# Kernel optimization log

Hardware: AMD Instinct MI355X
Metric: run time of the kernel (lower is better)

Reference implementation:

```python
import jax, jax.numpy as jnp
import numpy as np

N = 6144      # num_sample / nodes per graph
E = 196608    # edges per graph (avg degree 32)
F = 256       # input feature dim (same for all 4 graphs)
H = 256       # hidden_channels (== F so all SAGEConv layers are HxH)
D = 512       # fusion dim (hardcoded in module)
G = 4         # number of graphs
ATT = 128     # attention bottleneck (hardcoded)
WS = 0.05     # weight init scale


def setup_inputs() -> dict:
    key = jax.random.key(0)
    k = jax.random.split(key, 16)
    return {
        "xs": jax.random.normal(k[0], (G, N, F), jnp.float32),
        "edge_index": jax.random.randint(k[1], (G, 2, E), 0, N),
        "x_content": jax.random.normal(k[2], (N, F), jnp.float32),
        # SAGEConv params: per graph, 3 layers, lin_l (with bias) on aggregated
        # neighbors, lin_r (no bias) on root. F == H so all layers stack.
        "sage_Wl": jax.random.normal(k[3], (G, 3, H, H), jnp.float32) * WS,
        "sage_bl": jnp.zeros((G, 3, H), jnp.float32),
        "sage_Wr": jax.random.normal(k[4], (G, 3, H, H), jnp.float32) * WS,
        # lin1..lin4 : F -> 512
        "lin_W": jax.random.normal(k[5], (G, D, F), jnp.float32) * WS,
        "lin_b": jnp.zeros((G, D), jnp.float32),
        # ResidualFusion attention MLP 512 -> 128 -> 1, softmax over graph axis
        "att_W1": jax.random.normal(k[6], (ATT, D), jnp.float32) * WS,
        "att_b1": jnp.zeros((ATT,), jnp.float32),
        "att_W2": jax.random.normal(k[7], (1, ATT), jnp.float32) * WS,
        "att_b2": jnp.zeros((1,), jnp.float32),
        "res_W": jax.random.normal(k[8], (D, D), jnp.float32) * WS,
        "res_b": jnp.zeros((D,), jnp.float32),
        "fusion_weight": jnp.array([0.7, 0.3], jnp.float32),
        # SelfExpression coefficients, init 1e-8 * ones as in the module
        "C_content": jnp.full((N, N), 1e-8, jnp.float32),
        "C_structure": jnp.full((N, N), 1e-8, jnp.float32),
    }


def _gnn(x, ei, Wl, bl, Wr):
    # One GraphSAGE stack: 3 SAGEConv(mean) layers, relu after each,
    # dropout is identity in eval mode.
    src, dst = ei[0], ei[1]
    deg = jax.ops.segment_sum(jnp.ones((E,), x.dtype), dst, num_segments=N)
    deg = jnp.maximum(deg, 1.0)[:, None]
    for i in range(3):
        m = jax.ops.segment_sum(x[src], dst, num_segments=N) / deg  # mean aggr
        x = jax.nn.relu(m @ Wl[i].T + bl[i] + x @ Wr[i].T)
    return x


def reference(xs, edge_index, x_content, sage_Wl, sage_bl, sage_Wr,
              lin_W, lin_b, att_W1, att_b1, att_W2, att_b2,
              res_W, res_b, fusion_weight, C_content, C_structure):
    # Four GraphSAGE stacks, vmapped over the graph axis.
    xg = jax.vmap(_gnn)(xs, edge_index, sage_Wl, sage_bl, sage_Wr)  # [G,N,F]
    # lin1..lin4 -> [G,N,D]
    feats = jnp.einsum('gnf,gdf->gnd', xg, lin_W) + lin_b[:, None, :]
    # ResidualFusion: attention over stacked features, softmax over graph axis
    h = jax.nn.relu(jnp.einsum('gnd,kd->gnk', feats, att_W1) + att_b1)
    logits = jnp.einsum('gnk,ok->gno', h, att_W2) + att_b2  # [G,N,1]
    w = jax.nn.softmax(logits, axis=0)
    weighted = jnp.sum(w * feats, axis=0)            # [N,D]
    residual = feats[0] @ res_W.T + res_b            # [N,D]
    structure_features = jax.nn.relu(weighted + residual)
    # Coefficient fusion with softmax-normalized scalar weights
    fw = jax.nn.softmax(fusion_weight)
    fusion_expression = fw[0] * C_content + fw[1] * C_structure  # [N,N]
    return (fusion_expression, x_content, structure_features, C_content, C_structure)
```

## Files before the change

### kernel.cpp

```cpp
#include <hip/hip_runtime.h>
#include <hip/hip_bf16.h>

constexpr int N_ = 6144;
constexpr int E_ = 196608;
constexpr int F_ = 256;
constexpr int D_ = 512;
constexpr int G_ = 4;
constexpr int A_ = 128;

typedef short bf16x8 __attribute__((ext_vector_type(8)));
typedef float f32x4 __attribute__((ext_vector_type(4)));
typedef float f4 __attribute__((ext_vector_type(4)));
typedef int i4 __attribute__((ext_vector_type(4)));
typedef __hip_bfloat16 hb;

__device__ inline float b2f(unsigned short u) {
    union { unsigned u32; float f; } x; x.u32 = ((unsigned)u) << 16; return x.f;
}
__device__ inline unsigned short f2bu(float f) {
    hb b = __float2bfloat16(f);
    return *reinterpret_cast<unsigned short*>(&b);
}

#define GLD_LDS16(gp, lp) \
    __builtin_amdgcn_global_load_lds((const __attribute__((address_space(1))) void*)(gp), \
                                     (__attribute__((address_space(3))) void*)(lp), 16, 0, 0)

struct SP {
    const f4* Cc; const f4* Cs; const float* fw;
    f4* o0; f4* o3; f4* o4;
    long ib; long ie; int nsb;
};

__device__ void stream_slice(const SP sp, int sb)
{
    float fa = sp.fw[0], fb = sp.fw[1];
    float mx = fmaxf(fa, fb);
    float ea = expf(fa - mx), eb = expf(fb - mx);
    float w0 = ea / (ea + eb), w1 = eb / (ea + eb);
    const long S = (long)sp.nsb * blockDim.x;
    long i = sp.ib + (long)sb * blockDim.x + threadIdx.x;
    for (; i + 3 * S < sp.ie; i += 4 * S) {
        f4 a0 = __builtin_nontemporal_load(sp.Cc + i);
        f4 b0 = __builtin_nontemporal_load(sp.Cs + i);
        f4 a1 = __builtin_nontemporal_load(sp.Cc + i + S);
        f4 b1 = __builtin_nontemporal_load(sp.Cs + i + S);
        f4 a2 = __builtin_nontemporal_load(sp.Cc + i + 2 * S);
        f4 b2 = __builtin_nontemporal_load(sp.Cs + i + 2 * S);
        f4 a3 = __builtin_nontemporal_load(sp.Cc + i + 3 * S);
        f4 b3 = __builtin_nontemporal_load(sp.Cs + i + 3 * S);
        __builtin_nontemporal_store(a0, sp.o3 + i);
        __builtin_nontemporal_store(b0, sp.o4 + i);
        __builtin_nontemporal_store(w0 * a0 + w1 * b0, sp.o0 + i);
        __builtin_nontemporal_store(a1, sp.o3 + i + S);
        __builtin_nontemporal_store(b1, sp.o4 + i + S);
        __builtin_nontemporal_store(w0 * a1 + w1 * b1, sp.o0 + i + S);
        __builtin_nontemporal_store(a2, sp.o3 + i + 2 * S);
        __builtin_nontemporal_store(b2, sp.o4 + i + 2 * S);
        __builtin_nontemporal_store(w0 * a2 + w1 * b2, sp.o0 + i + 2 * S);
        __builtin_nontemporal_store(a3, sp.o3 + i + 3 * S);
        __builtin_nontemporal_store(b3, sp.o4 + i + 3 * S);
        __builtin_nontemporal_store(w0 * a3 + w1 * b3, sp.o0 + i + 3 * S);
    }
    for (; i < sp.ie; i += S) {
        f4 a = __builtin_nontemporal_load(sp.Cc + i);
        f4 b = __builtin_nontemporal_load(sp.Cs + i);
        __builtin_nontemporal_store(a, sp.o3 + i);
        __builtin_nontemporal_store(b, sp.o4 + i);
        __builtin_nontemporal_store(w0 * a + w1 * b, sp.o0 + i);
    }
}

__global__ void k_tail(SP sp) { stream_slice(sp, blockIdx.x); }

__global__ void k_prep(const float* __restrict__ xc, f4* __restrict__ o1,
                       const float* __restrict__ xs, ushort4* __restrict__ xsb,
                       const float* __restrict__ Wl, ushort4* __restrict__ Wlb,
                       const float* __restrict__ Wr, ushort4* __restrict__ Wrb,
                       const float* __restrict__ lin, ushort4* __restrict__ linb,
                       const float* __restrict__ aw, ushort4* __restrict__ awb,
                       const float* __restrict__ rw, ushort4* __restrict__ rwb,
                       i4* __restrict__ cursz, int PB, SP sp)
{
    if ((int)blockIdx.x < sp.nsb) { stream_slice(sp, blockIdx.x); return; }
    const int cb = blockIdx.x - sp.nsb;
    const long nz = (long)G_ * N_ / 4;
    const long n0 = (long)N_ * F_ / 4;
    const long n1 = (long)G_ * N_ * F_ / 4;
    const long n2 = (long)G_ * 3 * F_ * F_ / 4;
    const long n4 = (long)G_ * D_ * F_ / 4;
    const long n5 = (long)A_ * D_ / 4;
    const long n6 = (long)D_ * D_ / 4;
    const long T = nz + n0 + n1 + 2 * n2 + n4 + n5 + n6;
    long stride = (long)PB * blockDim.x;
    for (long u = (long)cb * blockDim.x + threadIdx.x; u < T; u += stride) {
        long v = u;
        if (v < nz) { cursz[v] = i4{0, 0, 0, 0}; continue; }
        v -= nz;
        if (v < n0) {
            f4 x = __builtin_nontemporal_load((const f4*)xc + v);
            __builtin_nontemporal_store(x, o1 + v);
            continue;
        }
        v -= n0;
        const float* s; ushort4* d;
        if (v < n1) { s = xs; d = xsb; }
        else {
            v -= n1;
            if (v < n2) { s = Wl; d = Wlb; }
            else {
                v -= n2;
                if (v < n2) { s = Wr; d = Wrb; }
                else {
                    v -= n2;
                    if (v < n4) { s = lin; d = linb; }
                    else {
                        v -= n4;
                        if (v < n5) { s = aw; d = awb; }
                        else { v -= n5; s = rw; d = rwb; }
                    }
                }
            }
        }
        f4 x = *((const f4*)s + v);
        ushort4 o;
        o.x = f2bu(x[0]); o.y = f2bu(x[1]); o.z = f2bu(x[2]); o.w = f2bu(x[3]);
        d[v] = o;
    }
}

__global__ void k_count(const int* __restrict__ ei, int* __restrict__ cnt, SP sp)
{
    if ((int)blockIdx.x < sp.nsb) { stream_slice(sp, blockIdx.x); return; }
    long i = (long)(blockIdx.x - sp.nsb) * blockDim.x + threadIdx.x;
    int g = (int)(i / E_);
    int e = (int)(i % E_);
    int dst = ei[(long)g * 2 * E_ + E_ + e];
    atomicAdd(&cnt[g * N_ + dst], 1);
}

__global__ void k_scan(int* __restrict__ cnt_cursor, int* __restrict__ row_ptr,
                       float* __restrict__ deg, SP sp)
{
    if ((int)blockIdx.x < sp.nsb) { stream_slice(sp, blockIdx.x); return; }
    int g = blockIdx.x - sp.nsb;
    __shared__ int sdata[1024];
    __shared__ int s_off;
    if (threadIdx.x == 0) s_off = 0;
    __syncthreads();
    for (int base = 0; base < N_; base += 1024) {
        int idx = g * N_ + base + threadIdx.x;
        int v = cnt_cursor[idx];
        sdata[threadIdx.x] = v;
        __syncthreads();
        for (int d = 1; d < 1024; d <<= 1) {
            int t = (threadIdx.x >= d) ? sdata[threadIdx.x - d] : 0;
            __syncthreads();
            sdata[threadIdx.x] += t;
            __syncthreads();
        }
        int incl = sdata[threadIdx.x];
        int excl = incl - v;
        int rp = s_off + excl;
        row_ptr[g * (N_ + 1) + base + threadIdx.x] = rp;
        cnt_cursor[idx] = rp;
        deg[idx] = (float)(v > 1 ? v : 1);
        __syncthreads();
        if (threadIdx.x == 1023) s_off += incl;
        __syncthreads();
    }
    if (threadIdx.x == 0) row_ptr[g * (N_ + 1) + N_] = s_off;
}

__global__ void k_fill(const int* __restrict__ ei, int* __restrict__ cursor,
                       int* __restrict__ csr_src, SP sp)
{
    if ((int)blockIdx.x < sp.nsb) { stream_slice(sp, blockIdx.x); return; }
    long i = (long)(blockIdx.x - sp.nsb) * blockDim.x + threadIdx.x;
    int g = (int)(i / E_);
    int e = (int)(i % E_);
    int src = ei[(long)g * 2 * E_ + e];
    int dst = ei[(long)g * 2 * E_ + E_ + e];
    int pos = atomicAdd(&cursor[g * N_ + dst], 1);
    csr_src[(long)g * E_ + pos] = src;
}

__global__ __launch_bounds__(256) void k_aggregate(
    const hb* __restrict__ x, const int* __restrict__ csr_src,
    const int* __restrict__ row_ptr, const float* __restrict__ deg,
    hb* __restrict__ m, SP sp)
{
    if ((int)blockIdx.x < sp.nsb) { stream_slice(sp, blockIdx.x); return; }
    int b = blockIdx.x - sp.nsb;
    int g = (b & 7) >> 1;
    int idx = ((b >> 3) << 1) | (b & 1);
    int node = idx * 4 + (threadIdx.x >> 6);
    int lane = threadIdx.x & 63;
    int qq = lane >> 4;
    int l16 = (lane & 15) * 16;
    const hb* xg = x + (long)g * N_ * F_;
    const int* rp = row_ptr + g * (N_ + 1);
    const int* cs = csr_src + (long)g * E_;
    int s = __builtin_amdgcn_readfirstlane(rp[node]);
    int e = __builtin_amdgcn_readfirstlane(rp[node + 1]);
    float a[16] = {};
    #pragma unroll 2
    for (int j = s; j < e; j += 4) {
        if (j + qq < e) {
            int src = cs[j + qq];
            const bf16x8* p = (const bf16x8*)(xg + (long)src * F_ + l16);
            bf16x8 v0 = p[0], v1 = p[1];
            #pragma unroll
            for (int q = 0; q < 8; ++q) a[q]     += b2f((unsigned short)v0[q]);
            #pragma unroll
            for (int q = 0; q < 8; ++q) a[q + 8] += b2f((unsigned short)v1[q]);
        }
    }
    #pragma unroll
    for (int q = 0; q < 16; ++q) {
        a[q] += __shfl_xor(a[q], 16);
        a[q] += __shfl_xor(a[q], 32);
    }
    if (qq == 0) {
        float inv = 1.0f / deg[g * N_ + node];
        bf16x8 lo, hi;
        #pragma unroll
        for (int q = 0; q < 8; ++q) { lo[q] = (short)f2bu(a[q] * inv); hi[q] = (short)f2bu(a[q + 8] * inv); }
        *(bf16x8*)(m + ((long)g * N_ + node) * F_ + l16) = lo;
        *(bf16x8*)(m + ((long)g * N_ + node) * F_ + l16 + 8) = hi;
    }
}

template <bool DUAL, bool RELU, bool LOGITS, bool FUSEOUT, bool PIN>
__global__ __launch_bounds__(256) void k_mfma_nt(
    const hb* __restrict__ A1, const hb* __restrict__ B1,
    const hb* __restrict__ A2, const hb* __restrict__ B2,
    const float* __restrict__ bias, hb* __restrict__ C,
    int ncols, int nrows, int ng, int Nc, int K,
    long a_batch, long b_batch, long bias_batch, long c_batch,
    const float* __restrict__ W2, const float* __restrict__ b2,
    float* __restrict__ logits,
    const float* __restrict__ lgAll, const hb* __restrict__ fAll,
    float* __restrict__ o2,
    SP sp)
{
    if ((int)blockIdx.x < sp.nsb) { stream_slice(sp, blockIdx.x); return; }
    int b = blockIdx.x - sp.nsb;
    int g, col, row;
    if (PIN) {
        g = (b & 7) >> 1;
        int idx = ((b >> 3) << 1) | (b & 1);
        col = idx % ncols; row = idx / ncols;
    } else {
        col = b % ncols;
        int r2 = b / ncols;
        row = r2 % nrows; g = r2 / nrows;
    }
    const int row0 = row * 128;
    const int col0 = col * 128;

    const hb* A1p = A1 + (long)g * a_batch;
    const hb* B1p = B1 + (long)g * b_batch;
    const hb* A2p = nullptr;
    const hb* B2p = nullptr;
    if (DUAL) { A2p = A2 + (long)g * a_batch; B2p = B2 + (long)g * b_batch; }
    const float* biasp = bias + (long)g * bias_batch;
    hb* Cp = C + (long)g * c_batch;

    __shared__ hb As[128 * 64];
    __shared__ hb Bs[128 * 64];
    __shared__ float sLog[2][128];
    __shared__ float sW[128][4];

    const int tid = threadIdx.x;
    const int lane = tid & 63;
    const int wid = tid >> 6;
    const int wr = wid >> 1;
    const int wc = wid & 1;

    if (FUSEOUT) {
        if (tid < 128) {
            int rr = row0 + tid;
            float l0 = lgAll[rr], l1 = lgAll[N_ + rr], l2 = lgAll[2 * N_ + rr], l3 = lgAll[3 * N_ + rr];
            float mx = fmaxf(fmaxf(l0, l1), fmaxf(l2, l3));
            float e0 = expf(l0 - mx), e1 = expf(l1 - mx), e2 = expf(l2 - mx), e3 = expf(l3 - mx);
            float inv = 1.f / (e0 + e1 + e2 + e3);
            sW[tid][0] = e0 * inv; sW[tid][1] = e1 * inv;
            sW[tid][2] = e2 * inv; sW[tid][3] = e3 * inv;
        }
    }

    const int srow = tid >> 3;
    const int sk8  = (tid & 7) * 8;

    f32x4 acc[4][4] = {};

    const int fr  = lane & 15;
    const int fkq = (lane >> 4) * 8;

    const int npass = DUAL ? 2 : 1;
    for (int pass = 0; pass < npass; ++pass) {
        const hb* A = (DUAL && pass) ? A2p : A1p;
        const hb* B = (DUAL && pass) ? B2p : B1p;
        for (int k0 = 0; k0 < K; k0 += 64) {
            __syncthreads();
            #pragma unroll
            for (int c = 0; c < 4; ++c) {
                int r = c * 32 + srow;
                GLD_LDS16(A + (long)(row0 + r) * K + k0 + sk8, As + r * 64 + sk8);
                GLD_LDS16(B + (long)(col0 + r) * K + k0 + sk8, Bs + r * 64 + sk8);
            }
            __syncthreads();

            bf16x8 af[4][2], bfr[4][2];
            #pragma unroll
            for (int m = 0; m < 4; ++m)
                #pragma unroll
                for (int kk = 0; kk < 2; ++kk)
                    af[m][kk] = *(const bf16x8*)(As + (wr * 64 + m * 16 + fr) * 64 + kk * 32 + fkq);
            #pragma unroll
            for (int n = 0; n < 4; ++n)
                #pragma unroll
                for (int kk = 0; kk < 2; ++kk)
                    bfr[n][kk] = *(const bf16x8*)(Bs + (wc * 64 + n * 16 + fr) * 64 + kk * 32 + fkq);

            #pragma unroll
            for (int m = 0; m < 4; ++m)
                #pragma unroll
                for (int n = 0; n < 4; ++n)
                    #pragma unroll
                    for (int kk = 0; kk < 2; ++kk)
                        acc[m][n] = __builtin_amdgcn_mfma_f32_16x16x32_bf16(
                            af[m][kk], bfr[n][kk], acc[m][n], 0, 0, 0);
        }
    }

    const int r4 = (lane >> 4) * 4;
    const int cc = lane & 15;

    if (LOGITS) {
        float w2v[4], bv[4];
        #pragma unroll
        for (int n = 0; n < 4; ++n) {
            int c2 = wc * 64 + n * 16 + cc;
            w2v[n] = W2[c2];
            bv[n]  = biasp[c2];
        }
        #pragma unroll
        for (int m = 0; m < 4; ++m) {
            #pragma unroll
            for (int j = 0; j < 4; ++j) {
                float p = 0.f;
                #pragma unroll
                for (int n = 0; n < 4; ++n) {
                    float h = fmaxf(acc[m][n][j] + bv[n], 0.f);
                    p += h * w2v[n];
                }
                p += __shfl_xor(p, 1); p += __shfl_xor(p, 2);
                p += __shfl_xor(p, 4); p += __shfl_xor(p, 8);
                if (cc == 0) sLog[wc][wr * 64 + m * 16 + r4 + j] = p;
            }
        }
        __syncthreads();
        if (tid < 128)
            logits[(long)g * N_ + row0 + tid] = sLog[0][tid] + sLog[1][tid] + b2[0];
    } else if (FUSEOUT) {
        const unsigned short* fu = (const unsigned short*)fAll;
        #pragma unroll
        for (int m = 0; m < 4; ++m) {
            #pragma unroll
            for (int n = 0; n < 4; ++n) {
                int c2 = col0 + wc * 64 + n * 16 + cc;
                float bv = biasp[c2];
                #pragma unroll
                for (int j = 0; j < 4; ++j) {
                    int rl = wr * 64 + m * 16 + r4 + j;
                    int rr = row0 + rl;
                    float s = acc[m][n][j] + bv;
                    #pragma unroll
                    for (int gg = 0; gg < 4; ++gg)
                        s += sW[rl][gg] * b2f(fu[((long)gg * N_ + rr) * D_ + c2]);
                    __builtin_nontemporal_store(fmaxf(s, 0.f), o2 + (long)rr * D_ + c2);
                }
            }
        }
    } else {
        #pragma unroll
        for (int m = 0; m < 4; ++m) {
            #pragma unroll
            for (int n = 0; n < 4; ++n) {
                int c2 = col0 + wc * 64 + n * 16 + cc;
                float bv = biasp[c2];
                #pragma unroll
                for (int j = 0; j < 4; ++j) {
                    int rr = row0 + wr * 64 + m * 16 + r4 + j;
                    float v = acc[m][n][j] + bv;
                    if (RELU) v = fmaxf(v, 0.f);
                    Cp[(long)rr * Nc + c2] = __float2bfloat16(v);
                }
            }
        }
    }
}

extern "C" void kernel_launch(void* const* d_in, const int* in_sizes, int n_in,
                              void* d_out, int out_size, void* d_ws, size_t ws_size,
                              hipStream_t stream)
{
    const float* xs        = (const float*)d_in[0];
    const int*   ei        = (const int*)  d_in[1];
    const float* x_content = (const float*)d_in[2];
    const float* sage_Wl   = (const float*)d_in[3];
    const float* sage_bl   = (const float*)d_in[4];
    const float* sage_Wr   = (const float*)d_in[5];
    const float* lin_W     = (const float*)d_in[6];
    const float* lin_b     = (const float*)d_in[7];
    const float* att_W1    = (const float*)d_in[8];
    const float* att_b1    = (const float*)d_in[9];
    const float* att_W2    = (const float*)d_in[10];
    const float* att_b2    = (const float*)d_in[11];
    const float* res_W     = (const float*)d_in[12];
    const float* res_b     = (const float*)d_in[13];
    const float* fusion_w  = (const float*)d_in[14];
    const float* Cc        = (const float*)d_in[15];
    const float* Cs        = (const float*)d_in[16];

    float* out0 = (float*)d_out;
    float* out1 = out0 + (size_t)N_ * N_;
    float* out2 = out1 + (size_t)N_ * F_;
    float* out3 = out2 + (size_t)N_ * D_;
    float* out4 = out3 + (size_t)N_ * N_;

    char* w = (char*)d_ws;
    auto alloc = [&](size_t bytes) {
        char* p = w;
        w += (bytes + 255) & ~(size_t)255;
        return p;
    };
    hb* xsb   = (hb*)alloc((size_t)G_ * N_ * F_ * 2);
    hb* xA    = (hb*)alloc((size_t)G_ * N_ * F_ * 2);
    hb* xB    = (hb*)alloc((size_t)G_ * N_ * F_ * 2);
    hb* mb    = (hb*)alloc((size_t)G_ * N_ * F_ * 2);
    hb* feats = (hb*)alloc((size_t)G_ * N_ * D_ * 2);
    hb* Wlb   = (hb*)alloc((size_t)G_ * 3 * F_ * F_ * 2);
    hb* Wrb   = (hb*)alloc((size_t)G_ * 3 * F_ * F_ * 2);
    hb* linWb = (hb*)alloc((size_t)G_ * D_ * F_ * 2);
    hb* attWb = (hb*)alloc((size_t)A_ * D_ * 2);
    hb* resWb = (hb*)alloc((size_t)D_ * D_ * 2);
    float* logit = (float*)alloc((size_t)G_ * N_ * 4);
    float* deg   = (float*)alloc((size_t)G_ * N_ * 4);
    int*   rowp  = (int*)  alloc((size_t)G_ * (N_ + 1) * 4);
    int*   curs  = (int*)  alloc((size_t)G_ * N_ * 4);
    int*   csrc  = (int*)  alloc((size_t)G_ * E_ * 4);

    const long U = (long)N_ * N_ / 4;
    const int cum[14] = {0, 85, 115, 135, 175, 285, 360, 470, 545, 655, 730, 820, 870, 975};
    long B[14];
    for (int i = 0; i < 14; ++i) B[i] = U * cum[i] / 1000;
    const int PREPB   = 512;
    const int SB_PREP = 512;
    const int SB_FLAT = 256;
    const int SB_GEMM = 256;
    const int TAILB   = 1024;
    auto mkSP = [&](int i, int nsb) {
        SP sp;
        sp.Cc = (const f4*)Cc; sp.Cs = (const f4*)Cs; sp.fw = fusion_w;
        sp.o0 = (f4*)out0; sp.o3 = (f4*)out3; sp.o4 = (f4*)out4;
        sp.ib = B[i]; sp.ie = (i == 13) ? U : B[i + 1]; sp.nsb = nsb;
        return sp;
    };
    SP tail = mkSP(13, TAILB);

    k_prep<<<SB_PREP + PREPB, 256, 0, stream>>>(
        x_content, (f4*)out1, xs, (ushort4*)xsb,
        sage_Wl, (ushort4*)Wlb, sage_Wr, (ushort4*)Wrb,
        lin_W, (ushort4*)linWb, att_W1, (ushort4*)attWb, res_W, (ushort4*)resWb,
        (i4*)curs, PREPB, mkSP(0, SB_PREP));

    k_count<<<SB_FLAT + G_ * E_ / 256, 256, 0, stream>>>(ei, curs, mkSP(1, SB_FLAT));
    k_scan<<<SB_FLAT + G_, 1024, 0, stream>>>(curs, rowp, deg, mkSP(2, SB_FLAT));
    k_fill<<<SB_FLAT + G_ * E_ / 256, 256, 0, stream>>>(ei, curs, csrc, mkSP(3, SB_FLAT));

    const hb* xin = xsb;
    hb* xout = xA;
    for (int layer = 0; layer < 3; ++layer) {
        k_aggregate<<<SB_FLAT + G_ * N_ / 4, 256, 0, stream>>>(
            xin, csrc, rowp, deg, mb, mkSP(4 + 2 * layer, SB_FLAT));
        k_mfma_nt<true, true, false, false, true>
            <<<SB_GEMM + (F_ / 128) * (N_ / 128) * G_, 256, 0, stream>>>(
            mb, Wlb + (size_t)layer * F_ * F_,
            xin, Wrb + (size_t)layer * F_ * F_,
            sage_bl + (size_t)layer * F_, xout,
            F_ / 128, N_ / 128, G_, F_, F_,
            (long)N_ * F_, (long)3 * F_ * F_, (long)3 * F_, (long)N_ * F_,
            nullptr, nullptr, nullptr, nullptr, nullptr, nullptr,
            mkSP(5 + 2 * layer, SB_GEMM));
        xin = xout;
        xout = (layer == 0) ? xB : xA;
    }
    const hb* xg = xA;

    k_mfma_nt<false, false, false, false, true>
        <<<SB_GEMM + (D_ / 128) * (N_ / 128) * G_, 256, 0, stream>>>(
        xg, linWb, nullptr, nullptr, lin_b, feats,
        D_ / 128, N_ / 128, G_, D_, F_,
        (long)N_ * F_, (long)D_ * F_, (long)D_, (long)N_ * D_,
        nullptr, nullptr, nullptr, nullptr, nullptr, nullptr,
        mkSP(10, SB_GEMM));

    k_mfma_nt<false, true, true, false, true>
        <<<SB_GEMM + (A_ / 128) * (N_ / 128) * G_, 256, 0, stream>>>(
        feats, attWb, nullptr, nullptr, att_b1, nullptr,
        A_ / 128, N_ / 128, G_, A_, D_,
        (long)N_ * D_, 0L, 0L, 0L,
        att_W2, att_b2, logit, nullptr, nullptr, nullptr,
        mkSP(11, SB_GEMM));

    k_mfma_nt<false, false, false, true, false>
        <<<SB_GEMM + (D_ / 128) * (N_ / 128) * 1, 256, 0, stream>>>(
        feats, resWb, nullptr, nullptr, res_b, nullptr,
        D_ / 128, N_ / 128, 1, D_, D_,
        0L, 0L, 0L, 0L,
        nullptr, nullptr, nullptr, logit, feats, out2,
        mkSP(12, SB_GEMM));

    k_tail<<<TAILB, 256, 0, stream>>>(tail);
}
```

Measured before the change: 428.0 us.

## Replace static stream slices with atomic work-stealing chunks fused into every kernel

The big C-matrix copy/blend stream was statically sliced across dedicated blocks in each launch. Each launch now owns a range of fixed-size chunks that blocks claim through a per-stage atomic cursor. Every compute block also joins the stream work after finishing its own task, which should fill idle CUs and balance the bandwidth-bound copy against the compute stages. This adds an atomic and two barriers per chunk, a memset launch, and relies on per-stage chunk counts that were picked by hand.

Result: slower. 651.1 us (+52.1%).

```diff
diff --git a/kernel.cpp b/kernel.cpp
--- a/kernel.cpp
+++ b/kernel.cpp
@@ -8,6 +8,10 @@
 constexpr int G_ = 4;
 constexpr int A_ = 128;
 
+constexpr int CHUNK = 4096;
+constexpr long U_F4 = (long)N_ * N_ / 4;
+constexpr int NCHUNKS = (int)(U_F4 / CHUNK);
+
 typedef short bf16x8 __attribute__((ext_vector_type(8)));
 typedef float f32x4 __attribute__((ext_vector_type(4)));
 typedef float f4 __attribute__((ext_vector_type(4)));
@@ -29,49 +33,52 @@
 struct SP {
     const f4* Cc; const f4* Cs; const float* fw;
     f4* o0; f4* o3; f4* o4;
-    long ib; long ie; int nsb;
+    int* cursor;
+    int cbeg; int cend;
 };
 
-__device__ void stream_slice(const SP sp, int sb)
-{
+__device__ void stream_steal(const SP sp)
+{
+    __shared__ int s_c;
     float fa = sp.fw[0], fb = sp.fw[1];
     float mx = fmaxf(fa, fb);
     float ea = expf(fa - mx), eb = expf(fb - mx);
     float w0 = ea / (ea + eb), w1 = eb / (ea + eb);
-    const long S = (long)sp.nsb * blockDim.x;
-    long i = sp.ib + (long)sb * blockDim.x + threadIdx.x;
-    for (; i + 3 * S < sp.ie; i += 4 * S) {
-        f4 a0 = __builtin_nontemporal_load(sp.Cc + i);
-        f4 b0 = __builtin_nontemporal_load(sp.Cs + i);
-        f4 a1 = __builtin_nontemporal_load(sp.Cc + i + S);
-        f4 b1 = __builtin_nontemporal_load(sp.Cs + i + S);
-        f4 a2 = __builtin_nontemporal_load(sp.Cc + i + 2 * S);
-        f4 b2 = __builtin_nontemporal_load(sp.Cs + i + 2 * S);
-        f4 a3 = __builtin_nontemporal_load(sp.Cc + i + 3 * S);
-        f4 b3 = __builtin_nontemporal_load(sp.Cs + i + 3 * S);
-        __builtin_nontemporal_store(a0, sp.o3 + i);
-        __builtin_nontemporal_store(b0, sp.o4 + i);
-        __builtin_nontemporal_store(w0 * a0 + w1 * b0, sp.o0 + i);
-        __builtin_nontemporal_store(a1, sp.o3 + i + S);
-        __builtin_nontemporal_store(b1, sp.o4 + i + S);
-        __builtin_nontemporal_store(w0 * a1 + w1 * b1, sp.o0 + i + S);
-        __builtin_nontemporal_store(a2, sp.o3 + i + 2 * S);
-        __builtin_nontemporal_store(b2, sp.o4 + i + 2 * S);
-        __builtin_nontemporal_store(w0 * a2 + w1 * b2, sp.o0 + i + 2 * S);
-        __builtin_nontemporal_store(a3, sp.o3 + i + 3 * S);
-        __builtin_nontemporal_store(b3, sp.o4 + i + 3 * S);
-        __builtin_nontemporal_store(w0 * a3 + w1 * b3, sp.o0 + i + 3 * S);
-    }
-    for (; i < sp.ie; i += S) {
-        f4 a = __builtin_nontemporal_load(sp.Cc + i);
-        f4 b = __builtin_nontemporal_load(sp.Cs + i);
-        __builtin_nontemporal_store(a, sp.o3 + i);
-        __builtin_nontemporal_store(b, sp.o4 + i);
-        __builtin_nontemporal_store(w0 * a + w1 * b, sp.o0 + i);
-    }
-}
-
-__global__ void k_tail(SP sp) { stream_slice(sp, blockIdx.x); }
+    const long S = blockDim.x;
+    while (true) {
+        __syncthreads();
+        if (threadIdx.x == 0) s_c = atomicAdd(sp.cursor, 1);
+        __syncthreads();
+        int c = sp.cbeg + s_c;
+        if (c >= sp.cend) return;
+        const long base = (long)c * CHUNK;
+        const long end  = base + CHUNK;
+        for (long i = base + threadIdx.x; i < end; i += 4 * S) {
+            f4 a0 = __builtin_nontemporal_load(sp.Cc + i);
+            f4 b0 = __builtin_nontemporal_load(sp.Cs + i);
+            f4 a1 = __builtin_nontemporal_load(sp.Cc + i + S);
+            f4 b1 = __builtin_nontemporal_load(sp.Cs + i + S);
+            f4 a2 = __builtin_nontemporal_load(sp.Cc + i + 2 * S);
+            f4 b2 = __builtin_nontemporal_load(sp.Cs + i + 2 * S);
+            f4 a3 = __builtin_nontemporal_load(sp.Cc + i + 3 * S);
+            f4 b3 = __builtin_nontemporal_load(sp.Cs + i + 3 * S);
+            __builtin_nontemporal_store(a0, sp.o3 + i);
+            __builtin_nontemporal_store(b0, sp.o4 + i);
+            __builtin_nontemporal_store(w0 * a0 + w1 * b0, sp.o0 + i);
+            __builtin_nontemporal_store(a1, sp.o3 + i + S);
+            __builtin_nontemporal_store(b1, sp.o4 + i + S);
+            __builtin_nontemporal_store(w0 * a1 + w1 * b1, sp.o0 + i + S);
+            __builtin_nontemporal_store(a2, sp.o3 + i + 2 * S);
+            __builtin_nontemporal_store(b2, sp.o4 + i + 2 * S);
+            __builtin_nontemporal_store(w0 * a2 + w1 * b2, sp.o0 + i + 2 * S);
+            __builtin_nontemporal_store(a3, sp.o3 + i + 3 * S);
+            __builtin_nontemporal_store(b3, sp.o4 + i + 3 * S);
+            __builtin_nontemporal_store(w0 * a3 + w1 * b3, sp.o0 + i + 3 * S);
+        }
+    }
+}
+
+__global__ void k_drain(SP sp) { stream_steal(sp); }
 
 __global__ void k_prep(const float* __restrict__ xc, f4* __restrict__ o1,
                        const float* __restrict__ xs, ushort4* __restrict__ xsb,
@@ -82,8 +89,9 @@
                        const float* __restrict__ rw, ushort4* __restrict__ rwb,
                        i4* __restrict__ cursz, int PB, SP sp)
 {
-    if ((int)blockIdx.x < sp.nsb) { stream_slice(sp, blockIdx.x); return; }
-    const int cb = blockIdx.x - sp.nsb;
+    if ((int)blockIdx.x >= sp.cbeg - sp.cbeg + 0 && (int)blockIdx.x < 0) {}
+    if ((int)blockIdx.x >= PB) { stream_steal(sp); return; }
+    const int cb = blockIdx.x;
     const long nz = (long)G_ * N_ / 4;
     const long n0 = (long)N_ * F_ / 4;
     const long n1 = (long)G_ * N_ * F_ / 4;
@@ -127,108 +135,118 @@
         o.x = f2bu(x[0]); o.y = f2bu(x[1]); o.z = f2bu(x[2]); o.w = f2bu(x[3]);
         d[v] = o;
     }
-}
-
-__global__ void k_count(const int* __restrict__ ei, int* __restrict__ cnt, SP sp)
-{
-    if ((int)blockIdx.x < sp.nsb) { stream_slice(sp, blockIdx.x); return; }
-    long i = (long)(blockIdx.x - sp.nsb) * blockDim.x + threadIdx.x;
-    int g = (int)(i / E_);
-    int e = (int)(i % E_);
-    int dst = ei[(long)g * 2 * E_ + E_ + e];
-    atomicAdd(&cnt[g * N_ + dst], 1);
+    stream_steal(sp);
+}
+
+__global__ void k_count(const int* __restrict__ ei, int* __restrict__ cnt,
+                        int nsb, SP sp)
+{
+    if ((int)blockIdx.x >= nsb) {
+        long i = (long)(blockIdx.x - nsb) * blockDim.x + threadIdx.x;
+        int g = (int)(i / E_);
+        int e = (int)(i % E_);
+        int dst = ei[(long)g * 2 * E_ + E_ + e];
+        atomicAdd(&cnt[g * N_ + dst], 1);
+    }
+    stream_steal(sp);
 }
 
 __global__ void k_scan(int* __restrict__ cnt_cursor, int* __restrict__ row_ptr,
-                       float* __restrict__ deg, SP sp)
-{
-    if ((int)blockIdx.x < sp.nsb) { stream_slice(sp, blockIdx.x); return; }
-    int g = blockIdx.x - sp.nsb;
-    __shared__ int sdata[1024];
-    __shared__ int s_off;
-    if (threadIdx.x == 0) s_off = 0;
-    __syncthreads();
-    for (int base = 0; base < N_; base += 1024) {
-        int idx = g * N_ + base + threadIdx.x;
-        int v = cnt_cursor[idx];
-        sdata[threadIdx.x] = v;
+                       float* __restrict__ deg, int nsb, SP sp)
+{
+    if ((int)blockIdx.x >= nsb) {
+        int g = blockIdx.x - nsb;
+        __shared__ int sdata[1024];
+        __shared__ int s_off;
+        if (threadIdx.x == 0) s_off = 0;
         __syncthreads();
-        for (int d = 1; d < 1024; d <<= 1) {
-            int t = (threadIdx.x >= d) ? sdata[threadIdx.x - d] : 0;
+        for (int base = 0; base < N_; base += 1024) {
+            int idx = g * N_ + base + threadIdx.x;
+            int v = cnt_cursor[idx];
+            sdata[threadIdx.x] = v;
             __syncthreads();
-            sdata[threadIdx.x] += t;
+            for (int d = 1; d < 1024; d <<= 1) {
+                int t = (threadIdx.x >= d) ? sdata[threadIdx.x - d] : 0;
+                __syncthreads();
+                sdata[threadIdx.x] += t;
+                __syncthreads();
+            }
+            int incl = sdata[threadIdx.x];
+            int excl = incl - v;
+            int rp = s_off + excl;
+            row_ptr[g * (N_ + 1) + base + threadIdx.x] = rp;
+            cnt_cursor[idx] = rp;
+            deg[idx] = (float)(v > 1 ? v : 1);
             __syncthreads();
-        }
-        int incl = sdata[threadIdx.x];
-        int excl = incl - v;
-        int rp = s_off + excl;
-        row_ptr[g * (N_ + 1) + base + threadIdx.x] = rp;
-        cnt_cursor[idx] = rp;
-        deg[idx] = (float)(v > 1 ? v : 1);
-        __syncthreads();
-        if (threadIdx.x == 1023) s_off += incl;
-        __syncthreads();
-    }
-    if (threadIdx.x == 0) row_ptr[g * (N_ + 1) + N_] = s_off;
+            if (threadIdx.x == 1023) s_off += incl;
+            __syncthreads();
+        }
+        if (threadIdx.x == 0) row_ptr[g * (N_ + 1) + N_] = s_off;
+    }
+    stream_steal(sp);
 }
 
 __global__ void k_fill(const int* __restrict__ ei, int* __restrict__ cursor,
-                       int* __restrict__ csr_src, SP sp)
-{
-    if ((int)blockIdx.x < sp.nsb) { stream_slice(sp, blockIdx.x); return; }
-    long i = (long)(blockIdx.x - sp.nsb) * blockDim.x + threadIdx.x;
-    int g = (int)(i / E_);
-    int e = (int)(i % E_);
-    int src = ei[(long)g * 2 * E_ + e];
-    int dst = ei[(long)g * 2 * E_ + E_ + e];
-    int pos = atomicAdd(&cursor[g * N_ + dst], 1);
-    csr_src[(long)g * E_ + pos] = src;
+                       int* __restrict__ csr_src, int nsb, SP sp)
+{
+    if ((int)blockIdx.x >= nsb) {
+        long i = (long)(blockIdx.x - nsb) * blockDim.x + threadIdx.x;
+        int g = (int)(i / E_);
+        int e = (int)(i % E_);
+        int src = ei[(long)g * 2 * E_ + e];
+        int dst = ei[(long)g * 2 * E_ + E_ + e];
+        int pos = atomicAdd(&cursor[g * N_ + dst], 1);
+        csr_src[(long)g * E_ + pos] = src;
+    }
+    stream_steal(sp);
 }
 
 __global__ __launch_bounds__(256) void k_aggregate(
     const hb* __restrict__ x, const int* __restrict__ csr_src,
     const int* __restrict__ row_ptr, const float* __restrict__ deg,
-    hb* __restrict__ m, SP sp)
-{
-    if ((int)blockIdx.x < sp.nsb) { stream_slice(sp, blockIdx.x); return; }
-    int b = blockIdx.x - sp.nsb;
-    int g = (b & 7) >> 1;
-    int idx = ((b >> 3) << 1) | (b & 1);
-    int node = idx * 4 + (threadIdx.x >> 6);
-    int lane = threadIdx.x & 63;
-    int qq = lane >> 4;
-    int l16 = (lane & 15) * 16;
-    const hb* xg = x + (long)g * N_ * F_;
-    const int* rp = row_ptr + g * (N_ + 1);
-    const int* cs = csr_src + (long)g * E_;
-    int s = __builtin_amdgcn_readfirstlane(rp[node]);
-    int e = __builtin_amdgcn_readfirstlane(rp[node + 1]);
-    float a[16] = {};
-    #pragma unroll 2
-    for (int j = s; j < e; j += 4) {
-        if (j + qq < e) {
-            int src = cs[j + qq];
-            const bf16x8* p = (const bf16x8*)(xg + (long)src * F_ + l16);
-            bf16x8 v0 = p[0], v1 = p[1];
-            #pragma unroll
-            for (int q = 0; q < 8; ++q) a[q]     += b2f((unsigned short)v0[q]);
-            #pragma unroll
-            for (int q = 0; q < 8; ++q) a[q + 8] += b2f((unsigned short)v1[q]);
-        }
-    }
-    #pragma unroll
-    for (int q = 0; q < 16; ++q) {
-        a[q] += __shfl_xor(a[q], 16);
-        a[q] += __shfl_xor(a[q], 32);
-    }
-    if (qq == 0) {
-        float inv = 1.0f / deg[g * N_ + node];
-        bf16x8 lo, hi;
+    hb* __restrict__ m, int nsb, SP sp)
+{
+    if ((int)blockIdx.x >= nsb) {
+        int b = blockIdx.x - nsb;
+        int g = (b & 7) >> 1;
+        int idx = ((b >> 3) << 1) | (b & 1);
+        int node = idx * 4 + (threadIdx.x >> 6);
+        int lane = threadIdx.x & 63;
+        int qq = lane >> 4;
+        int l16 = (lane & 15) * 16;
+        const hb* xg = x + (long)g * N_ * F_;
+        const int* rp = row_ptr + g * (N_ + 1);
+        const int* cs = csr_src + (long)g * E_;
+        int s = __builtin_amdgcn_readfirstlane(rp[node]);
+        int e = __builtin_amdgcn_readfirstlane(rp[node + 1]);
+        float a[16] = {};
+        #pragma unroll 2
+        for (int j = s; j < e; j += 4) {
+            if (j + qq < e) {
+                int src = cs[j + qq];
+                const bf16x8* p = (const bf16x8*)(xg + (long)src * F_ + l16);
+                bf16x8 v0 = p[0], v1 = p[1];
+                #pragma unroll
+                for (int q = 0; q < 8; ++q) a[q]     += b2f((unsigned short)v0[q]);
+                #pragma unroll
+                for (int q = 0; q < 8; ++q) a[q + 8] += b2f((unsigned short)v1[q]);
+            }
+        }
         #pragma unroll
-        for (int q = 0; q < 8; ++q) { lo[q] = (short)f2bu(a[q] * inv); hi[q] = (short)f2bu(a[q + 8] * inv); }
-        *(bf16x8*)(m + ((long)g * N_ + node) * F_ + l16) = lo;
-        *(bf16x8*)(m + ((long)g * N_ + node) * F_ + l16 + 8) = hi;
-    }
+        for (int q = 0; q < 16; ++q) {
+            a[q] += __shfl_xor(a[q], 16);
+            a[q] += __shfl_xor(a[q], 32);
+        }
+        if (qq == 0) {
+            float inv = 1.0f / deg[g * N_ + node];
+            bf16x8 lo, hi;
+            #pragma unroll
+            for (int q = 0; q < 8; ++q) { lo[q] = (short)f2bu(a[q] * inv); hi[q] = (short)f2bu(a[q + 8] * inv); }
+            *(bf16x8*)(m + ((long)g * N_ + node) * F_ + l16) = lo;
+            *(bf16x8*)(m + ((long)g * N_ + node) * F_ + l16 + 8) = hi;
+        }
+    }
+    stream_steal(sp);
 }
 
 template <bool DUAL, bool RELU, bool LOGITS, bool FUSEOUT, bool PIN>
@@ -242,10 +260,10 @@
     float* __restrict__ logits,
     const float* __restrict__ lgAll, const hb* __restrict__ fAll,
     float* __restrict__ o2,
-    SP sp)
-{
-    if ((int)blockIdx.x < sp.nsb) { stream_slice(sp, blockIdx.x); return; }
-    int b = blockIdx.x - sp.nsb;
+    int nsb, SP sp)
+{
+    if ((int)blockIdx.x >= nsb) {
+    int b = blockIdx.x - nsb;
     int g, col, row;
     if (PIN) {
         g = (b & 7) >> 1;
@@ -401,6 +419,8 @@
             }
         }
     }
+    }
+    stream_steal(sp);
 }
 
 extern "C" void kernel_launch(void* const* d_in, const int* in_sizes, int n_in,
@@ -452,77 +472,79 @@
     int*   rowp  = (int*)  alloc((size_t)G_ * (N_ + 1) * 4);
     int*   curs  = (int*)  alloc((size_t)G_ * N_ * 4);
     int*   csrc  = (int*)  alloc((size_t)G_ * E_ * 4);
-
-    const long U = (long)N_ * N_ / 4;
-    const int cum[14] = {0, 85, 115, 135, 175, 285, 360, 470, 545, 655, 730, 820, 870, 975};
-    long B[14];
-    for (int i = 0; i < 14; ++i) B[i] = U * cum[i] / 1000;
-    const int PREPB   = 512;
-    const int SB_PREP = 512;
-    const int SB_FLAT = 256;
-    const int SB_GEMM = 256;
-    const int TAILB   = 1024;
-    auto mkSP = [&](int i, int nsb) {
+    int*   scur  = (int*)  alloc(256);
+
+    const int chunks[14] = {256, 96, 32, 96, 160, 128, 160, 128, 160, 128, 128, 256, 320, 256};
+    int cb[15];
+    cb[0] = 0;
+    for (int i = 0; i < 14; ++i) cb[i + 1] = cb[i] + chunks[i];
+    auto mkSP = [&](int i) {
         SP sp;
         sp.Cc = (const f4*)Cc; sp.Cs = (const f4*)Cs; sp.fw = fusion_w;
         sp.o0 = (f4*)out0; sp.o3 = (f4*)out3; sp.o4 = (f4*)out4;
-        sp.ib = B[i]; sp.ie = (i == 13) ? U : B[i + 1]; sp.nsb = nsb;
+        sp.cursor = scur + i; sp.cbeg = cb[i]; sp.cend = cb[i + 1];
         return sp;
     };
-    SP tail = mkSP(13, TAILB);
-
-    k_prep<<<SB_PREP + PREPB, 256, 0, stream>>>(
+
+    const int PREPB = 1024;
+    const int SEED_P = 512;
+    const int SEED   = 256;
+    const int SEED_S = 64;
+
+    hipMemsetAsync(scur, 0, 64, stream);
+
+    k_prep<<<PREPB + SEED_P, 256, 0, stream>>>(
         x_content, (f4*)out1, xs, (ushort4*)xsb,
         sage_Wl, (ushort4*)Wlb, sage_Wr, (ushort4*)Wrb,
         lin_W, (ushort4*)linWb, att_W1, (ushort4*)attWb, res_W, (ushort4*)resWb,
-        (i4*)curs, PREPB, mkSP(0, SB_PREP));
-
-    k_count<<<SB_FLAT + G_ * E_ / 256, 256, 0, stream>>>(ei, curs, mkSP(1, SB_FLAT));
-    k_scan<<<SB_FLAT + G_, 1024, 0, stream>>>(curs, rowp, deg, mkSP(2, SB_FLAT));
-    k_fill<<<SB_FLAT + G_ * E_ / 256, 256, 0, stream>>>(ei, curs, csrc, mkSP(3, SB_FLAT));
+        (i4*)curs, PREPB, mkSP(0));
+
+    k_count<<<SEED + G_ * E_ / 256, 256, 0, stream>>>(ei, curs, SEED, mkSP(1));
+    k_scan<<<SEED_S + G_, 1024, 0, stream>>>(curs, rowp, deg, SEED_S, mkSP(2));
+    k_fill<<<SEED + G_ * E_ / 256, 256, 0, stream>>>(ei, curs, csrc, SEED, mkSP(3));
 
     const hb* xin = xsb;
     hb* xout = xA;
     for (int layer = 0; layer < 3; ++layer) {
-        k_aggregate<<<SB_FLAT + G_ * N_ / 4, 256, 0, stream>>>(
-            xin, csrc, rowp, deg, mb, mkSP(4 + 2 * layer, SB_FLAT));
+        k_aggregate<<<SEED + G_ * N_ / 4, 256, 0, stream>>>(
+            xin, csrc, rowp, deg, mb, SEED, mkSP(4 + 2 * layer));
         k_mfma_nt<true, true, false, false, true>
-            <<<SB_GEMM + (F_ / 128) * (N_ / 128) * G_, 256, 0, stream>>>(
+            <<<SEED + (F_ / 128) * (N_ / 128) * G_, 256, 0, stream>>>(
             mb, Wlb + (size_t)layer * F_ * F_,
             xin, Wrb + (size_t)layer * F_ * F_,
             sage_bl + (size_t)layer * F_, xout,
             F_ / 128, N_ / 128, G_, F_, F_,
             (long)N_ * F_, (long)3 * F_ * F_, (long)3 * F_, (long)N_ * F_,
             nullptr, nullptr, nullptr, nullptr, nullptr, nullptr,
-            mkSP(5 + 2 * layer, SB_GEMM));
+            SEED, mkSP(5 + 2 * layer));
         xin = xout;
         xout = (layer == 0) ? xB : xA;
     }
     const hb* xg = xA;
 
     k_mfma_nt<false, false, false, false, true>
-        <<<SB_GEMM + (D_ / 128) * (N_ / 128) * G_, 256, 0, stream>>>(
+        <<<SEED + (D_ / 128) * (N_ / 128) * G_, 256, 0, stream>>>(
         xg, linWb, nullptr, nullptr, lin_b, feats,
         D_ / 128, N_ / 128, G_, D_, F_,
         (long)N_ * F_, (long)D_ * F_, (long)D_, (long)N_ * D_,
         nullptr, nullptr, nullptr, nullptr, nullptr, nullptr,
-        mkSP(10, SB_GEMM));
+        SEED, mkSP(10));
 
     k_mfma_nt<false, true, true, false, true>
-        <<<SB_GEMM + (A_ / 128) * (N_ / 128) * G_, 256, 0, stream>>>(
+        <<<SEED_P + (A_ / 128) * (N_ / 128) * G_, 256, 0, stream>>>(
         feats, attWb, nullptr, nullptr, att_b1, nullptr,
         A_ / 128, N_ / 128, G_, A_, D_,
         (long)N_ * D_, 0L, 0L, 0L,
         att_W2, att_b2, logit, nullptr, nullptr, nullptr,
-        mkSP(11, SB_GEMM));
+        SEED_P, mkSP(11));
 
     k_mfma_nt<false, false, false, true, false>
-        <<<SB_GEMM + (D_ / 128) * (N_ / 128) * 1, 256, 0, stream>>>(
+        <<<SEED_P + (D_ / 128) * (N_ / 128) * 1, 256, 0, stream>>>(
         feats, resWb, nullptr, nullptr, res_b, nullptr,
         D_ / 128, N_ / 128, 1, D_, D_,
         0L, 0L, 0L, 0L,
         nullptr, nullptr, nullptr, logit, feats, out2,
-        mkSP(12, SB_GEMM));
-
-    k_tail<<<TAILB, 256, 0, stream>>>(tail);
-}
+        SEED_P, mkSP(12));
+
+    k_drain<<<1024, 256, 0, stream>>>(mkSP(13));
+}
```
